# Performance work log

Measured on AMD Instinct MI355X. Metric: run time of the kernel, lower is better.

The kernel has to match this reference:

```python
import jax, jax.numpy as jnp
import numpy as np
from itertools import combinations

B, F, C, MAX_ORDER = 4096, 32, 128, 3


def setup_inputs() -> dict:
    key = jax.random.key(0)
    ks = jax.random.split(key, 1 + MAX_ORDER)
    x = jax.random.normal(ks[0], (B, F), dtype=jnp.float32)
    # Exact combinatorial index lists, matching get_index_lists (all k-subsets, lexicographic)
    idx = [jnp.asarray(np.array(list(combinations(range(F), o)), dtype=np.int32))
           for o in range(1, MAX_ORDER + 1)]
    # Per-order Dense kernels [n_combos, num_classes] (glorot-ish scale), no bias (use_bias=False)
    Ws = [jax.random.normal(ks[i + 1], (idx[i].shape[0], C), dtype=jnp.float32)
          * (2.0 / (idx[i].shape[0] + C)) ** 0.5 for i in range(MAX_ORDER)]
    bias = jnp.zeros((1, C), dtype=jnp.float32)  # Zeros initializer
    return {"x": x, "bias": bias,
            "W1": Ws[0], "W2": Ws[1], "W3": Ws[2],
            "idx1": idx[0], "idx2": idx[1], "idx3": idx[2]}


def reference(x, bias, W1, W2, W3, idx1, idx2, idx3):
    # combine(): out = tile(bias) + sum_i Dense_i( prod over feature-subset of order i )
    out = jnp.broadcast_to(bias, (x.shape[0], bias.shape[1]))
    for idx, W in ((idx1, W1), (idx2, W2), (idx3, W3)):
        # x[:, idx]: [B, n_combos, order] gather; product over subset axis -> [B, n_combos]
        prods = jnp.prod(x[:, idx], axis=2)
        out = out + prods @ W  # [B, num_classes]
    return out
```

## Files before the change

### kernel.cpp

```cpp
#include <hip/hip_runtime.h>
#include <hip/hip_bf16.h>

constexpr int B_   = 4096;
constexpr int C_   = 128;
constexpr int K1   = 32;
constexpr int K2   = 496;
constexpr int K3   = 4960;
constexpr int KTOT = K1 + K2 + K3;
constexpr int KPAD = 5632;

constexpr int NCHUNK = KPAD / 16;
constexpr int WCH    = NCHUNK / 4;

typedef __attribute__((ext_vector_type(8)))  short bf16x8;
typedef __attribute__((ext_vector_type(16))) float f32x16;

constexpr size_t WS_WT = 0;

struct Sched { short a[KPAD]; short b[KPAD]; short c[KPAD]; };
constexpr Sched make_sched() {
    Sched s{}; int k = 0;
    for (int i = 0; i < 32; ++i) { s.a[k] = i; s.b[k] = 32; s.c[k] = 32; ++k; }
    for (int i = 0; i < 32; ++i)
        for (int j = i + 1; j < 32; ++j) { s.a[k] = i; s.b[k] = j; s.c[k] = 32; ++k; }
    for (int i = 0; i < 32; ++i)
        for (int j = i + 1; j < 32; ++j)
            for (int l = j + 1; l < 32; ++l) { s.a[k] = i; s.b[k] = j; s.c[k] = l; ++k; }
    for (; k < KPAD; ++k) { s.a[k] = 32; s.b[k] = 32; s.c[k] = 32; }
    return s;
}
constexpr Sched SCH = make_sched();

template<int K>
__device__ __forceinline__ float prodK(const float (&xv)[33]) {
    return xv[SCH.a[K]] * xv[SCH.b[K]] * xv[SCH.c[K]];
}

template<int K0, int J>
__device__ __forceinline__ void prods8(const float (&xv)[33], bool hi, float (&q)[8]) {
    if constexpr (J < 8) {
        q[J] = hi ? prodK<K0 + 8 + J>(xv) : prodK<K0 + J>(xv);
        prods8<K0, J + 1>(xv, hi, q);
    }
}

template<int WV, int CH>
__device__ __forceinline__ void run_chunks(const float (&xv)[33], bool hi, int lane, int ct,
                                           const ushort* __restrict__ Wb, f32x16& acc) {
    if constexpr (CH < WCH) {
        constexpr int G  = WV * WCH + CH;
        constexpr int K0 = G * 16;
        bf16x8 b0 = *(const bf16x8*)(Wb + ((size_t)(G * 4 + ct) * 64 + lane) * 8);
        float q[8];
        prods8<K0, 0>(xv, hi, q);
        union { ushort us[8]; bf16x8 v; } af;
        #pragma unroll
        for (int j = 0; j < 8; ++j) {
            __hip_bfloat16 h = __float2bfloat16(q[j]);
            af.us[j] = *reinterpret_cast<ushort*>(&h);
        }
        acc = __builtin_amdgcn_mfma_f32_32x32x16_bf16(af.v, b0, acc, 0, 0, 0);
        run_chunks<WV, CH + 1>(xv, hi, lane, ct, Wb, acc);
    }
}

__global__ __launch_bounds__(256)
void prep_wt(const float* __restrict__ W1,
             const float* __restrict__ W2,
             const float* __restrict__ W3,
             ushort* __restrict__ Wb)
{
    __shared__ ushort tile[16 * 130];
    const int gc = blockIdx.x, t = threadIdx.x;
    const int k0 = gc * 16;
    #pragma unroll
    for (int p = 0; p < 2; ++p) {
        int e  = p * 256 + t;
        int kk = e >> 5, cq = e & 31;
        int k  = k0 + kk;
        float4 v = {0.f, 0.f, 0.f, 0.f};
        if (k < K1)           v = ((const float4*)W1)[k * 32 + cq];
        else if (k < K1 + K2) v = ((const float4*)W2)[(k - K1) * 32 + cq];
        else if (k < KTOT)    v = ((const float4*)W3)[(k - K1 - K2) * 32 + cq];
        union { ushort u[4]; uint2 d; } o;
        __hip_bfloat16 h0 = __float2bfloat16(v.x); o.u[0] = *(ushort*)&h0;
        __hip_bfloat16 h1 = __float2bfloat16(v.y); o.u[1] = *(ushort*)&h1;
        __hip_bfloat16 h2 = __float2bfloat16(v.z); o.u[2] = *(ushort*)&h2;
        __hip_bfloat16 h3 = __float2bfloat16(v.w); o.u[3] = *(ushort*)&h3;
        *(uint2*)&tile[kk * 130 + cq * 4] = o.d;
    }
    __syncthreads();
    {
        int ct = t >> 6, lane = t & 63, n = lane & 31, kg = lane >> 5;
        union { ushort us[8]; uint4 d; } o;
        #pragma unroll
        for (int j = 0; j < 8; ++j) o.us[j] = tile[(kg * 8 + j) * 130 + ct * 32 + n];
        *(uint4*)&Wb[((size_t)(gc * 4 + ct) * 64 + lane) * 8] = o.d;
    }
}

__global__ __launch_bounds__(256, 2)
void poly_mfma(const float* __restrict__ x,
               const ushort* __restrict__ Wb,
               const float* __restrict__ bias,
               float* __restrict__ out)
{
    __shared__ float red[4][32 * 33];

    const int t    = threadIdx.x;
    const int lane = t & 63;
    const int w    = t >> 6;
    const int m    = lane & 31;
    const bool hi  = lane >= 32;
    const int row0 = blockIdx.x * 32;
    const int ct   = blockIdx.y;

    float xv[33];
    {
        const float4* xrow = (const float4*)(x + (size_t)(row0 + m) * 32);
        #pragma unroll
        for (int qv = 0; qv < 8; ++qv) {
            float4 v = xrow[qv];
            xv[qv * 4 + 0] = v.x; xv[qv * 4 + 1] = v.y;
            xv[qv * 4 + 2] = v.z; xv[qv * 4 + 3] = v.w;
        }
        xv[32] = 1.0f;
    }

    f32x16 acc;
    #pragma unroll
    for (int i = 0; i < 16; ++i) acc[i] = 0.f;

    switch (w) {
        case 0:  run_chunks<0, 0>(xv, hi, lane, ct, Wb, acc); break;
        case 1:  run_chunks<1, 0>(xv, hi, lane, ct, Wb, acc); break;
        case 2:  run_chunks<2, 0>(xv, hi, lane, ct, Wb, acc); break;
        default: run_chunks<3, 0>(xv, hi, lane, ct, Wb, acc); break;
    }

    const int kg = hi ? 1 : 0;
    #pragma unroll
    for (int e = 0; e < 16; ++e) {
        int r = (e & 3) + 8 * (e >> 2) + 4 * kg;
        red[w][r * 33 + m] = acc[e];
    }
    __syncthreads();

    {
        int r  = t >> 3;
        int c0 = (t & 7) * 4;
        float4 b = *(const float4*)&bias[ct * 32 + c0];
        float s[4] = {b.x, b.y, b.z, b.w};
        #pragma unroll
        for (int wv = 0; wv < 4; ++wv)
            #pragma unroll
            for (int j = 0; j < 4; ++j)
                s[j] += red[wv][r * 33 + c0 + j];
        float4 o = {s[0], s[1], s[2], s[3]};
        *(float4*)&out[(size_t)(row0 + r) * C_ + ct * 32 + c0] = o;
    }
}

extern "C" void kernel_launch(void* const* d_in, const int* in_sizes, int n_in,
                              void* d_out, int out_size, void* d_ws, size_t ws_size,
                              hipStream_t stream)
{
    const float* x    = (const float*)d_in[0];
    const float* bias = (const float*)d_in[1];
    const float* W1   = (const float*)d_in[2];
    const float* W2   = (const float*)d_in[3];
    const float* W3   = (const float*)d_in[4];
    float* out = (float*)d_out;

    ushort* Wb = (ushort*)((char*)d_ws + WS_WT);

    prep_wt<<<KPAD / 16, 256, 0, stream>>>(W1, W2, W3, Wb);

    dim3 grid(B_ / 32, C_ / 32);
    poly_mfma<<<grid, 256, 0, stream>>>(x, Wb, bias, out);
}
```

Baseline: 83.26 us.

## Split K across blocks with partial buffers and separate reduction kernel

Before, each block handled one 32-column class tile and its four waves split the K dimension, then reduced through shared memory. Now each block handles one quarter of K and its four waves cover the four 32-column tiles. Each wave writes its partial result to a workspace buffer, and a new kernel sums the four partials and adds the bias. This lets the four waves in a block share the same product terms across all output columns. The cost is an extra kernel launch plus a round trip of partial sums through global memory.

New measurement: 89.14 us. 1.07x slower.

```diff
diff --git a/kernel.cpp b/kernel.cpp
--- a/kernel.cpp
+++ b/kernel.cpp
@@ -10,12 +10,14 @@
 constexpr int KPAD = 5632;
 
 constexpr int NCHUNK = KPAD / 16;
-constexpr int WCH    = NCHUNK / 4;
+constexpr int NQ     = 4;
+constexpr int QCH    = NCHUNK / NQ;
 
 typedef __attribute__((ext_vector_type(8)))  short bf16x8;
 typedef __attribute__((ext_vector_type(16))) float f32x16;
 
-constexpr size_t WS_WT = 0;
+constexpr size_t WS_WT   = 0;
+constexpr size_t WS_PART = 2ull << 20;
 
 struct Sched { short a[KPAD]; short b[KPAD]; short c[KPAD]; };
 constexpr Sched make_sched() {
@@ -44,11 +46,11 @@
     }
 }
 
-template<int WV, int CH>
+template<int Q, int CH>
 __device__ __forceinline__ void run_chunks(const float (&xv)[33], bool hi, int lane, int ct,
                                            const ushort* __restrict__ Wb, f32x16& acc) {
-    if constexpr (CH < WCH) {
-        constexpr int G  = WV * WCH + CH;
+    if constexpr (CH < QCH) {
+        constexpr int G  = Q * QCH + CH;
         constexpr int K0 = G * 16;
         bf16x8 b0 = *(const bf16x8*)(Wb + ((size_t)(G * 4 + ct) * 64 + lane) * 8);
         float q[8];
@@ -60,7 +62,7 @@
             af.us[j] = *reinterpret_cast<ushort*>(&h);
         }
         acc = __builtin_amdgcn_mfma_f32_32x32x16_bf16(af.v, b0, acc, 0, 0, 0);
-        run_chunks<WV, CH + 1>(xv, hi, lane, ct, Wb, acc);
+        run_chunks<Q, CH + 1>(xv, hi, lane, ct, Wb, acc);
     }
 }
 
@@ -102,18 +104,14 @@
 __global__ __launch_bounds__(256, 2)
 void poly_mfma(const float* __restrict__ x,
                const ushort* __restrict__ Wb,
-               const float* __restrict__ bias,
-               float* __restrict__ out)
+               float* __restrict__ part)
 {
-    __shared__ float red[4][32 * 33];
-
     const int t    = threadIdx.x;
     const int lane = t & 63;
     const int w    = t >> 6;
     const int m    = lane & 31;
     const bool hi  = lane >= 32;
     const int row0 = blockIdx.x * 32;
-    const int ct   = blockIdx.y;
 
     float xv[33];
     {
@@ -131,34 +129,37 @@
     #pragma unroll
     for (int i = 0; i < 16; ++i) acc[i] = 0.f;
 
-    switch (w) {
-        case 0:  run_chunks<0, 0>(xv, hi, lane, ct, Wb, acc); break;
-        case 1:  run_chunks<1, 0>(xv, hi, lane, ct, Wb, acc); break;
-        case 2:  run_chunks<2, 0>(xv, hi, lane, ct, Wb, acc); break;
-        default: run_chunks<3, 0>(xv, hi, lane, ct, Wb, acc); break;
+    switch (blockIdx.y) {
+        case 0:  run_chunks<0, 0>(xv, hi, lane, w, Wb, acc); break;
+        case 1:  run_chunks<1, 0>(xv, hi, lane, w, Wb, acc); break;
+        case 2:  run_chunks<2, 0>(xv, hi, lane, w, Wb, acc); break;
+        default: run_chunks<3, 0>(xv, hi, lane, w, Wb, acc); break;
     }
 
     const int kg = hi ? 1 : 0;
+    float* base = part + (((size_t)blockIdx.y * B_ + row0) * C_ + w * 32);
     #pragma unroll
     for (int e = 0; e < 16; ++e) {
         int r = (e & 3) + 8 * (e >> 2) + 4 * kg;
-        red[w][r * 33 + m] = acc[e];
+        base[(size_t)r * C_ + m] = acc[e];
     }
-    __syncthreads();
+}
 
-    {
-        int r  = t >> 3;
-        int c0 = (t & 7) * 4;
-        float4 b = *(const float4*)&bias[ct * 32 + c0];
-        float s[4] = {b.x, b.y, b.z, b.w};
-        #pragma unroll
-        for (int wv = 0; wv < 4; ++wv)
-            #pragma unroll
-            for (int j = 0; j < 4; ++j)
-                s[j] += red[wv][r * 33 + c0 + j];
-        float4 o = {s[0], s[1], s[2], s[3]};
-        *(float4*)&out[(size_t)(row0 + r) * C_ + ct * 32 + c0] = o;
+__global__ __launch_bounds__(256)
+void reduce_out(const float* __restrict__ part,
+                const float* __restrict__ bias,
+                float* __restrict__ out)
+{
+    const int idx = blockIdx.x * 256 + threadIdx.x;
+    const int r   = idx >> 5;
+    const int c   = (idx & 31) * 4;
+    float4 s = *(const float4*)&bias[c];
+    #pragma unroll
+    for (int y = 0; y < NQ; ++y) {
+        float4 v = *(const float4*)&part[((size_t)y * B_ + r) * C_ + c];
+        s.x += v.x; s.y += v.y; s.z += v.z; s.w += v.w;
     }
+    *(float4*)&out[(size_t)r * C_ + c] = s;
 }
 
 extern "C" void kernel_launch(void* const* d_in, const int* in_sizes, int n_in,
@@ -170,12 +171,15 @@
     const float* W1   = (const float*)d_in[2];
     const float* W2   = (const float*)d_in[3];
     const float* W3   = (const float*)d_in[4];
-    float* out = (float*)d_out;
 
-    ushort* Wb = (ushort*)((char*)d_ws + WS_WT);
+    float* out  = (float*)d_out;
+    ushort* Wb  = (ushort*)((char*)d_ws + WS_WT);
+    float*  prt = (float*)((char*)d_ws + WS_PART);
 
-    prep_wt<<<KPAD / 16, 256, 0, stream>>>(W1, W2, W3, Wb);
+    prep_wt<<<NCHUNK, 256, 0, stream>>>(W1, W2, W3, Wb);
 
-    dim3 grid(B_ / 32, C_ / 32);
-    poly_mfma<<<grid, 256, 0, stream>>>(x, Wb, bias, out);
+    dim3 grid(B_ / 32, NQ);
+    poly_mfma<<<grid, 256, 0, stream>>>(x, Wb, prt);
+
+    reduce_out<<<(B_ * C_ / 4) / 256, 256, 0, stream>>>(prt, bias, out);
 }
```

## Prefetch weight fragments four chunks ahead and split MFMA accumulators

Applied to the files above, without the earlier changes.

Weight fragments for the MFMA are now software-prefetched four chunks ahead through a register rotation, so global load latency is hidden behind the product computation. The MFMA accumulation alternates between two accumulators to break the serial dependency chain, and the two are summed before the reduction. The x rows are staged through shared memory with a coalesced load instead of per-lane strided loads. This raises register pressure (extra fragments plus a second 16-float accumulator), which could hurt occupancy under the two-blocks-per-SM launch bound.

After: 80.96 us. -2.8%, faster.

```diff
diff --git a/kernel.cpp b/kernel.cpp
--- a/kernel.cpp
+++ b/kernel.cpp
@@ -44,24 +44,31 @@
     }
 }
 
+__device__ __forceinline__ bf16x8 ldb(const ushort* __restrict__ Wb, int G4ct, int lane) {
+    return *(const bf16x8*)(Wb + ((size_t)G4ct * 64 + lane) * 8);
+}
+
 template<int WV, int CH>
 __device__ __forceinline__ void run_chunks(const float (&xv)[33], bool hi, int lane, int ct,
-                                           const ushort* __restrict__ Wb, f32x16& acc) {
-    if constexpr (CH < WCH) {
-        constexpr int G  = WV * WCH + CH;
-        constexpr int K0 = G * 16;
-        bf16x8 b0 = *(const bf16x8*)(Wb + ((size_t)(G * 4 + ct) * 64 + lane) * 8);
-        float q[8];
-        prods8<K0, 0>(xv, hi, q);
-        union { ushort us[8]; bf16x8 v; } af;
-        #pragma unroll
-        for (int j = 0; j < 8; ++j) {
-            __hip_bfloat16 h = __float2bfloat16(q[j]);
-            af.us[j] = *reinterpret_cast<ushort*>(&h);
-        }
-        acc = __builtin_amdgcn_mfma_f32_32x32x16_bf16(af.v, b0, acc, 0, 0, 0);
-        run_chunks<WV, CH + 1>(xv, hi, lane, ct, Wb, acc);
-    }
+                                           const ushort* __restrict__ Wb,
+                                           bf16x8 b0, bf16x8 b1, bf16x8 b2, bf16x8 b3,
+                                           f32x16& a0, f32x16& a1) {
+    constexpr int G  = WV * WCH + CH;
+    constexpr int K0 = G * 16;
+    bf16x8 b4;
+    if constexpr (CH + 4 < WCH) b4 = ldb(Wb, (G + 4) * 4 + ct, lane);
+    float q[8];
+    prods8<K0, 0>(xv, hi, q);
+    union { ushort us[8]; bf16x8 v; } af;
+    #pragma unroll
+    for (int j = 0; j < 8; ++j) {
+        __hip_bfloat16 h = __float2bfloat16(q[j]);
+        af.us[j] = *reinterpret_cast<ushort*>(&h);
+    }
+    if constexpr (CH & 1) a1 = __builtin_amdgcn_mfma_f32_32x32x16_bf16(af.v, b0, a1, 0, 0, 0);
+    else                  a0 = __builtin_amdgcn_mfma_f32_32x32x16_bf16(af.v, b0, a0, 0, 0, 0);
+    if constexpr (CH + 1 < WCH)
+        run_chunks<WV, CH + 1>(xv, hi, lane, ct, Wb, b1, b2, b3, b4, a0, a1);
 }
 
 __global__ __launch_bounds__(256)
@@ -105,6 +112,7 @@
                const float* __restrict__ bias,
                float* __restrict__ out)
 {
+    __shared__ float xs[32 * 36];
     __shared__ float red[4][32 * 33];
 
     const int t    = threadIdx.x;
@@ -115,34 +123,45 @@
     const int row0 = blockIdx.x * 32;
     const int ct   = blockIdx.y;
 
+    {
+        float4 v = ((const float4*)(x + (size_t)row0 * 32))[t];
+        *(float4*)&xs[(t >> 3) * 36 + (t & 7) * 4] = v;
+    }
+    __syncthreads();
+
     float xv[33];
-    {
-        const float4* xrow = (const float4*)(x + (size_t)(row0 + m) * 32);
-        #pragma unroll
-        for (int qv = 0; qv < 8; ++qv) {
-            float4 v = xrow[qv];
-            xv[qv * 4 + 0] = v.x; xv[qv * 4 + 1] = v.y;
-            xv[qv * 4 + 2] = v.z; xv[qv * 4 + 3] = v.w;
-        }
-        xv[32] = 1.0f;
-    }
-
-    f32x16 acc;
-    #pragma unroll
-    for (int i = 0; i < 16; ++i) acc[i] = 0.f;
+    #pragma unroll
+    for (int qv = 0; qv < 8; ++qv) {
+        float4 v = *(const float4*)&xs[m * 36 + qv * 4];
+        xv[qv * 4 + 0] = v.x; xv[qv * 4 + 1] = v.y;
+        xv[qv * 4 + 2] = v.z; xv[qv * 4 + 3] = v.w;
+    }
+    xv[32] = 1.0f;
+
+    f32x16 a0, a1;
+    #pragma unroll
+    for (int i = 0; i < 16; ++i) { a0[i] = 0.f; a1[i] = 0.f; }
 
     switch (w) {
-        case 0:  run_chunks<0, 0>(xv, hi, lane, ct, Wb, acc); break;
-        case 1:  run_chunks<1, 0>(xv, hi, lane, ct, Wb, acc); break;
-        case 2:  run_chunks<2, 0>(xv, hi, lane, ct, Wb, acc); break;
-        default: run_chunks<3, 0>(xv, hi, lane, ct, Wb, acc); break;
+#define RUNW(WV) { \
+        constexpr int G0 = WV * WCH; \
+        bf16x8 b0 = ldb(Wb, (G0 + 0) * 4 + ct, lane); \
+        bf16x8 b1 = ldb(Wb, (G0 + 1) * 4 + ct, lane); \
+        bf16x8 b2 = ldb(Wb, (G0 + 2) * 4 + ct, lane); \
+        bf16x8 b3 = ldb(Wb, (G0 + 3) * 4 + ct, lane); \
+        run_chunks<WV, 0>(xv, hi, lane, ct, Wb, b0, b1, b2, b3, a0, a1); }
+        case 0:  RUNW(0) break;
+        case 1:  RUNW(1) break;
+        case 2:  RUNW(2) break;
+        default: RUNW(3) break;
+#undef RUNW
     }
 
     const int kg = hi ? 1 : 0;
     #pragma unroll
     for (int e = 0; e < 16; ++e) {
         int r = (e & 3) + 8 * (e >> 2) + 4 * kg;
-        red[w][r * 33 + m] = acc[e];
+        red[w][r * 33 + m] = a0[e] + a1[e];
     }
     __syncthreads();
 
@@ -174,7 +193,7 @@
 
     ushort* Wb = (ushort*)((char*)d_ws + WS_WT);
 
-    prep_wt<<<KPAD / 16, 256, 0, stream>>>(W1, W2, W3, Wb);
+    prep_wt<<<NCHUNK, 256, 0, stream>>>(W1, W2, W3, Wb);
 
     dim3 grid(B_ / 32, C_ / 32);
     poly_mfma<<<grid, 256, 0, stream>>>(x, Wb, bias, out);
```
